# Kernel tuning notes

Measured on AMD Instinct MI355X. Metric: run time of the kernel, lower is better.

The kernel has to match this reference:

```python
import jax, jax.numpy as jnp
import numpy as np

VAR = (0.1, 0.2)        # SSD encoding variances
THRESH = 0.5            # overlap_thresh
NEGPOS = 3              # neg:pos ratio


def _point_form(p):
    # (cx,cy,w,h) -> (x1,y1,x2,y2)
    return jnp.concatenate([p[:, :2] - p[:, 2:] / 2, p[:, :2] + p[:, 2:] / 2], axis=1)


def _jaccard(a, b):
    # a: [O,4], b: [P,4], corner form -> IoU [O,P]
    lt = jnp.maximum(a[:, None, :2], b[None, :, :2])
    rb = jnp.minimum(a[:, None, 2:], b[None, :, 2:])
    wh = jnp.maximum(rb - lt, 0.0)
    inter = wh[..., 0] * wh[..., 1]
    area_a = ((a[:, 2] - a[:, 0]) * (a[:, 3] - a[:, 1]))[:, None]
    area_b = ((b[:, 2] - b[:, 0]) * (b[:, 3] - b[:, 1]))[None, :]
    return inter / (area_a + area_b - inter)


def _encode(matched, priors):
    # matched: [P,4] corner form, priors: [P,4] center form
    g_cxcy = ((matched[:, :2] + matched[:, 2:]) / 2 - priors[:, :2]) / (VAR[0] * priors[:, 2:])
    g_wh = jnp.log((matched[:, 2:] - matched[:, :2]) / priors[:, 2:]) / VAR[1]
    return jnp.concatenate([g_cxcy, g_wh], axis=1)


def _match(truths, labels, priors):
    # truths: [O,4], labels: [O], priors: [P,4] -> loc_t [P,4], conf_t [P], obj_t [P]
    O = truths.shape[0]
    over = _jaccard(truths, _point_form(priors))          # [O,P]
    best_prior_idx = jnp.argmax(over, axis=1)             # [O] best prior per truth
    best_truth_overlap = over.max(axis=0)                 # [P]
    best_truth_idx = jnp.argmax(over, axis=0)             # [P]
    best_truth_overlap = best_truth_overlap.at[best_prior_idx].set(2.0)
    best_truth_idx = best_truth_idx.at[best_prior_idx].set(jnp.arange(O))
    matched = truths[best_truth_idx]                      # [P,4]
    conf = labels[best_truth_idx].astype(jnp.int32) + 1   # background = 0
    conf = jnp.where(best_truth_overlap < THRESH, 0, conf)
    return _encode(matched, priors), conf, conf > 0


def _ce(logits, tgt):
    # per-element cross entropy, logits [...,C], tgt [...] int
    return jax.nn.logsumexp(logits, axis=-1) - jnp.take_along_axis(logits, tgt[..., None], axis=-1)[..., 0]


def _mine_neg(loss, pos, P):
    # hard negative mining via double argsort (rank of each elem in descending loss order)
    loss = jnp.where(pos, 0.0, loss)
    loss_idx = jnp.argsort(-loss, axis=1)
    idx_rank = jnp.argsort(loss_idx, axis=1)
    num_neg = jnp.minimum(NEGPOS * pos.sum(axis=1, keepdims=True), P - 1)
    return idx_rank < num_neg


def setup_inputs() -> dict:
    key = jax.random.key(0)
    ks = jax.random.split(key, 8)
    B, P, C, O = 64, 16320, 81, 50
    loc_data = jax.random.normal(ks[0], (B, P, 4), jnp.float32)
    conf_data = jax.random.normal(ks[1], (B, P, C), jnp.float32)
    obj_data = jax.random.normal(ks[2], (B, P, 2), jnp.float32)
    # priors: center form, positive w/h
    cxcy = jax.random.uniform(ks[3], (P, 2), minval=0.05, maxval=0.95)
    wh = jax.random.uniform(ks[4], (P, 2), minval=0.02, maxval=0.3)
    priors = jnp.concatenate([cxcy, wh], axis=1).astype(jnp.float32)
    # targets: valid corner-form boxes + float label in last column
    tc = jax.random.uniform(ks[5], (B, O, 2), minval=0.1, maxval=0.9)
    twh = jax.random.uniform(ks[6], (B, O, 2), minval=0.05, maxval=0.3)
    boxes = jnp.concatenate([jnp.clip(tc - twh / 2, 0.0, 1.0), jnp.clip(tc + twh / 2, 0.0, 1.0)], axis=-1)
    labels = jax.random.randint(ks[7], (B, O), 0, C).astype(jnp.float32)
    targets = jnp.concatenate([boxes, labels[..., None]], axis=-1).astype(jnp.float32)
    return {"loc_data": loc_data, "conf_data": conf_data, "obj_data": obj_data,
            "priors": priors, "targets": targets}


def reference(loc_data, conf_data, obj_data, priors, targets):
    B, P, C = conf_data.shape
    loc_t, conf_t, pos = jax.vmap(lambda t: _match(t[:, :4], t[:, 4], priors))(targets)
    loc_t = jax.lax.stop_gradient(loc_t)  # torch builds targets detached

    # localization: smooth L1 over positives, sum reduction
    d = loc_data - loc_t
    sl1 = jnp.where(jnp.abs(d) < 1.0, 0.5 * d * d, jnp.abs(d) - 0.5)
    loss_l = jnp.sum(sl1 * pos[..., None].astype(sl1.dtype))

    # combined (C+1)-way logit: col0 = obj_bg + log(sum(exp(conf))), cols 1..C = obj_fg + conf
    lse_conf = jax.nn.logsumexp(conf_data, axis=-1)                        # [B,P]
    logit = jnp.concatenate([(obj_data[..., 0] + lse_conf)[..., None],
                             obj_data[..., 1:2] + conf_data], axis=-1)     # [B,P,C+1]

    ce_c = _ce(logit, conf_t)                       # [B,P]
    neg_c = _mine_neg(ce_c, pos, P)
    loss_c = jnp.sum(jnp.where(pos | neg_c, ce_c, 0.0))

    ce_o = _ce(obj_data, pos.astype(jnp.int32))     # [B,P]
    neg_o = _mine_neg(ce_o, pos, P)
    loss_obj = jnp.sum(jnp.where(pos | neg_o, ce_o, 0.0))

    N = pos.sum().astype(jnp.float32)
    return loss_l / N, loss_c / N, loss_obj / N
```

## Files before the change

### kernel.cpp

```cpp
#include <hip/hip_runtime.h>
#include <cstdint>
#include <cstddef>

#define THRESH   0.5f
#define NEGPOS   3
#define VAR0     0.1f
#define VAR1     0.2f
#define MAXO     64
#define NPRI     8
#define A1_T     256
#define MINE_T   1024
#define MINE_W   (MINE_T / 64)
#define HCOPIES  8

__global__ __launch_bounds__(A1_T)
void match_kernel(const float* __restrict__ priors,
                  const float* __restrict__ targets,
                  unsigned char* __restrict__ code,
                  unsigned long long* __restrict__ g_bp,
                  int B, int P, int O, int chunks) {
    __shared__ float tx1[MAXO], ty1[MAXO], tx2[MAXO], ty2[MAXO], tarea[MAXO];
    const int b   = blockIdx.x / chunks;
    const int ch  = blockIdx.x % chunks;
    const int tid = threadIdx.x;

    if (tid < O) {
        const float* tr = targets + (size_t)(b * O + tid) * 5;
        float x1 = tr[0], y1 = tr[1], x2 = tr[2], y2 = tr[3];
        tx1[tid] = x1; ty1[tid] = y1; tx2[tid] = x2; ty2[tid] = y2;
        tarea[tid] = (x2 - x1) * (y2 - y1);
    }
    __syncthreads();

    float px1[NPRI], py1[NPRI], px2[NPRI], py2[NPRI], pa[NPRI], pov[NPRI];
    int   pidx[NPRI];
    const int p0 = ch * (A1_T * NPRI) + tid;
#pragma unroll
    for (int i = 0; i < NPRI; ++i) {
        int p = p0 + i * A1_T;
        pov[i] = -1.0f; pidx[i] = 0;
        px1[i] = 0.f; py1[i] = 0.f; px2[i] = 0.f; py2[i] = 0.f; pa[i] = 1.0f;
        if (p < P) {
            float4 pr = *(const float4*)(priors + (size_t)p * 4);
            px1[i] = pr.x - pr.z * 0.5f; py1[i] = pr.y - pr.w * 0.5f;
            px2[i] = pr.x + pr.z * 0.5f; py2[i] = pr.y + pr.w * 0.5f;
            pa[i]  = pr.z * pr.w;
        }
    }

    const int lane = tid & 63;
    for (int o = 0; o < O; ++o) {
        float ax1 = tx1[o], ay1 = ty1[o], ax2 = tx2[o], ay2 = ty2[o], aa = tarea[o];
        float bo = -1.0f; unsigned bp = 0u;
#pragma unroll
        for (int i = 0; i < NPRI; ++i) {
            float lx = fmaxf(ax1, px1[i]), ly = fmaxf(ay1, py1[i]);
            float rx = fminf(ax2, px2[i]), ry = fminf(ay2, py2[i]);
            float w = fmaxf(rx - lx, 0.0f), h = fmaxf(ry - ly, 0.0f);
            float inter = w * h;
            float iou = __fdividef(inter, aa + pa[i] - inter);
            if (iou > pov[i]) { pov[i] = iou; pidx[i] = o; }
            if (iou > bo)     { bo = iou; bp = (unsigned)(p0 + i * A1_T); }
        }
        unsigned long long key =
            ((unsigned long long)__float_as_uint(bo) << 32) |
            (unsigned long long)(0xFFFFFFFFu - bp);
#pragma unroll
        for (int d = 1; d < 64; d <<= 1) {
            unsigned long long other = __shfl_xor(key, d, 64);
            if (other > key) key = other;
        }
        if (lane == 0)
            atomicMax(&g_bp[(size_t)b * O + o], key);
    }

#pragma unroll
    for (int i = 0; i < NPRI; ++i) {
        int p = p0 + i * A1_T;
        if (p < P)
            code[(size_t)b * P + p] =
                (pov[i] >= THRESH) ? (unsigned char)(pidx[i] + 1) : (unsigned char)0;
    }
}

__global__ void force_kernel(const unsigned long long* __restrict__ g_bp,
                             unsigned char* __restrict__ code,
                             int B, int P, int O) {
    int b = blockIdx.x * blockDim.x + threadIdx.x;
    if (b >= B) return;
    for (int o = 0; o < O; ++o) {
        unsigned long long key = g_bp[(size_t)b * O + o];
        unsigned p = 0xFFFFFFFFu - (unsigned)(key & 0xFFFFFFFFull);
        code[(size_t)b * P + p] = (unsigned char)(o + 1);
    }
}

__global__ __launch_bounds__(256)
void ce_pos_kernel(const float* __restrict__ loc, const float* __restrict__ conf,
                   const float* __restrict__ obj, const float* __restrict__ priors,
                   const float* __restrict__ targets,
                   const unsigned char* __restrict__ code,
                   float* __restrict__ mce, float* __restrict__ rowacc,
                   int B, int P, int C, int O) {
    const int b = blockIdx.y;
    const int p = blockIdx.x * 256 + threadIdx.x;
    const int tid = threadIdx.x, wv = tid >> 6, lane = tid & 63;

    bool pos = false;
    unsigned cc = 0;
    const unsigned t = (unsigned)(b * P + p);
    float obx = 0.f, oby = 0.f, lse2 = 0.f;
    if (p < P) {
        cc = code[t];
        float2 ob = *(const float2*)(obj + (size_t)t * 2);
        obx = ob.x; oby = ob.y;
        float m = fmaxf(obx, oby);
        lse2 = m + __logf(__expf(obx - m) + __expf(oby - m));
        if (cc == 0) {
            mce[t] = lse2 - obx;
        } else {
            mce[t] = 0.0f;
            pos = true;
        }
    }

    const unsigned long long msk = __ballot(pos);
    float myS = 0.f;
    unsigned long long rem = msk;
    while (rem) {
        const int src = __ffsll(rem) - 1;
        rem &= rem - 1;
        const unsigned t_s = (unsigned)__shfl((int)t, src, 64);
        const float* cr = conf + (size_t)t_s * C;
        float s = 0.f;
        for (int j = lane; j < C; j += 64) s += __expf(cr[j]);
#pragma unroll
        for (int d = 1; d < 64; d <<= 1) s += __shfl_xor(s, d, 64);
        if (lane == src) myS = s;
    }

    float sl = 0.f, cec = 0.f, ceo = 0.f;
    if (pos) {
        const float* cr = conf + (size_t)t * C;
        const float* tr = targets + (size_t)((unsigned)(b * O) + cc - 1u) * 5;
        float4 pr = *(const float4*)(priors + (size_t)p * 4);
        float4 ld = *(const float4*)(loc + (size_t)t * 4);
        float mx1 = tr[0], my1 = tr[1], mx2 = tr[2], my2 = tr[3];
        int   lbl = (int)tr[4];

        float lsec = __logf(myS);
        cec = lsec + lse2 - oby - cr[lbl];
        ceo = lse2 - oby;

        float gx  = ((mx1 + mx2) * 0.5f - pr.x) / (VAR0 * pr.z);
        float gy  = ((my1 + my2) * 0.5f - pr.y) / (VAR0 * pr.w);
        float gw2 = __logf((mx2 - mx1) / pr.z) / VAR1;
        float gh  = __logf((my2 - my1) / pr.w) / VAR1;
        float d0 = ld.x - gx,  a0 = fabsf(d0); sl += (a0 < 1.f) ? 0.5f * d0 * d0 : a0 - 0.5f;
        float d1 = ld.y - gy,  a1 = fabsf(d1); sl += (a1 < 1.f) ? 0.5f * d1 * d1 : a1 - 0.5f;
        float d2 = ld.z - gw2, a2 = fabsf(d2); sl += (a2 < 1.f) ? 0.5f * d2 * d2 : a2 - 0.5f;
        float d3 = ld.w - gh,  a3 = fabsf(d3); sl += (a3 < 1.f) ? 0.5f * d3 * d3 : a3 - 0.5f;
    }

    float cntp = (float)__popcll(msk);
    __shared__ float red[4][4];
#pragma unroll
    for (int d = 32; d > 0; d >>= 1) {
        sl  += __shfl_down(sl,  d, 64);
        cec += __shfl_down(cec, d, 64);
        ceo += __shfl_down(ceo, d, 64);
    }
    if (lane == 0) {
        red[wv][0] = cntp; red[wv][1] = sl; red[wv][2] = cec; red[wv][3] = ceo;
    }
    __syncthreads();
    if (tid < 4) {
        float v = red[0][tid] + red[1][tid] + red[2][tid] + red[3][tid];
        if (v != 0.0f)
            atomicAdd(rowacc + (size_t)b * 16 + tid, v);
    }
}

__global__ __launch_bounds__(MINE_T)
void mine_kernel(const float* __restrict__ mce, const float* __restrict__ rowacc,
                 float* __restrict__ g_neg, int P) {
    const int b = blockIdx.x;
    const float* row = mce + (size_t)b * P;
    int npos = (int)rowacc[(size_t)b * 16];
    int k = NEGPOS * npos;
    if (k > P - 1) k = P - 1;
    if (k <= 0) return;

    __shared__ unsigned hist[HCOPIES][257];
    __shared__ unsigned s_prefix;
    __shared__ int      s_rem;
    __shared__ float    s_ws[MINE_W];
    __shared__ int      s_wc[MINE_W];

    const int tid  = threadIdx.x;
    const int wv   = tid >> 6;
    const int hc   = wv & (HCOPIES - 1);
    const int lane = tid & 63;

    unsigned prefix = 0u;
    int rem = k;
    for (int shift = 24; shift >= 0; shift -= 8) {
        for (int i = tid; i < HCOPIES * 257; i += MINE_T) (&hist[0][0])[i] = 0u;
        __syncthreads();
        unsigned himask = (shift == 24) ? 0u : (0xFFFFFFFFu << (shift + 8));
        for (int i = tid; i < P; i += MINE_T) {
            unsigned bits = __float_as_uint(row[i]);
            if ((bits & himask) == prefix)
                atomicAdd(&hist[hc][(bits >> shift) & 0xFFu], 1u);
        }
        __syncthreads();
        if (tid == 0) {
            int cum = 0; unsigned bin = 0;
            for (int bb = 255; bb >= 0; --bb) {
                int cnt = 0;
#pragma unroll
                for (int h = 0; h < HCOPIES; ++h) cnt += (int)hist[h][bb];
                if (cum + cnt >= rem) { bin = (unsigned)bb; rem -= cum; break; }
                cum += cnt;
            }
            s_prefix = prefix | (bin << shift);
            s_rem = rem;
        }
        __syncthreads();
        prefix = s_prefix;
        rem    = s_rem;
    }

    float vk = __uint_as_float(prefix);
    float s = 0.f; int cnt = 0;
    for (int i = tid; i < P; i += MINE_T) {
        float v = row[i];
        if (__float_as_uint(v) > prefix) { s += v; ++cnt; }
    }
#pragma unroll
    for (int d = 32; d > 0; d >>= 1) {
        s   += __shfl_down(s, d, 64);
        cnt += __shfl_down(cnt, d, 64);
    }
    if (lane == 0) { s_ws[wv] = s; s_wc[wv] = cnt; }
    __syncthreads();
    if (tid == 0) {
        float st = 0.f; int ct = 0;
        for (int w = 0; w < MINE_W; ++w) { st += s_ws[w]; ct += s_wc[w]; }
        atomicAdd(g_neg, st + (float)(k - ct) * vk);
    }
}

__global__ void finish_kernel(const float* __restrict__ rowacc,
                              const float* __restrict__ g_neg,
                              float* __restrict__ out, int B) {
    const int lane = threadIdx.x;
    float npos = 0.f, sl = 0.f, cec = 0.f, ceo = 0.f;
    for (int b = lane; b < B; b += 64) {
        float4 v = *(const float4*)(rowacc + (size_t)b * 16);
        npos += v.x; sl += v.y; cec += v.z; ceo += v.w;
    }
#pragma unroll
    for (int d = 32; d > 0; d >>= 1) {
        npos += __shfl_down(npos, d, 64);
        sl   += __shfl_down(sl,   d, 64);
        cec  += __shfl_down(cec,  d, 64);
        ceo  += __shfl_down(ceo,  d, 64);
    }
    if (lane == 0) {
        float neg = *g_neg;
        out[0] = sl / npos;
        out[1] = (cec + neg) / npos;
        out[2] = (ceo + neg) / npos;
    }
}

extern "C" void kernel_launch(void* const* d_in, const int* in_sizes, int n_in,
                              void* d_out, int out_size, void* d_ws, size_t ws_size,
                              hipStream_t stream) {
    const float* loc     = (const float*)d_in[0];
    const float* conf    = (const float*)d_in[1];
    const float* obj     = (const float*)d_in[2];
    const float* priors  = (const float*)d_in[3];
    const float* targets = (const float*)d_in[4];

    const int P = in_sizes[3] / 4;
    const int B = in_sizes[0] / (4 * P);
    const int C = in_sizes[1] / (B * P);
    const int O = in_sizes[4] / (5 * B);

    char* ws = (char*)d_ws;
    size_t off = 0;
    float* g_neg = (float*)(ws + off);             off += 64;
    float* rowacc = (float*)(ws + off);            off += (size_t)B * 16 * sizeof(float);
    unsigned long long* g_bp = (unsigned long long*)(ws + off);
    off += (size_t)B * O * sizeof(unsigned long long);
    const size_t zero_bytes = off;
    off = (off + 127) & ~(size_t)127;
    unsigned char* code = (unsigned char*)(ws + off); off += (size_t)B * P;
    off = (off + 127) & ~(size_t)127;
    float* mce = (float*)(ws + off);               off += (size_t)B * P * sizeof(float);

    hipMemsetAsync(d_ws, 0, zero_bytes, stream);

    const int chunks = (P + A1_T * NPRI - 1) / (A1_T * NPRI);
    match_kernel<<<B * chunks, A1_T, 0, stream>>>(priors, targets, code, g_bp,
                                                  B, P, O, chunks);
    force_kernel<<<(B + 63) / 64, 64, 0, stream>>>(g_bp, code, B, P, O);
    dim3 ce_grid((P + 255) / 256, B);
    ce_pos_kernel<<<ce_grid, 256, 0, stream>>>(loc, conf, obj, priors, targets,
                                               code, mce, rowacc, B, P, C, O);
    mine_kernel<<<B, MINE_T, 0, stream>>>(mce, rowacc, g_neg, P);
    finish_kernel<<<1, 64, 0, stream>>>(rowacc, g_neg, (float*)d_out, B);
}
```

Before: 587.5 us.

## Fuse CE/positive pass with hard-negative mining in one per-row block

Merges the per-prior cross-entropy/positive-loss kernel and the radix-select mining kernel into one kernel with one 1024-thread block per batch row, keeping the mined losses in registers instead of writing and rereading them from global memory. It also parallelizes the force-match step per target with duplicate resolution, and replaces the serial bin scan in the radix select with a wave prefix scan. Per-row results go straight into rowacc instead of through atomics. The cost is much less parallelism in the CE stage (B blocks instead of B×P/256), and it caps P at 16K priors per row.

```diff
diff --git a/kernel.cpp b/kernel.cpp
--- a/kernel.cpp
+++ b/kernel.cpp
@@ -9,9 +9,9 @@
 #define MAXO     64
 #define NPRI     8
 #define A1_T     256
-#define MINE_T   1024
-#define MINE_W   (MINE_T / 64)
-#define HCOPIES  8
+#define FUSED_T  1024
+#define FWAVES   (FUSED_T / 64)
+#define MAXCH    16
 
 __global__ __launch_bounds__(A1_T)
 void match_kernel(const float* __restrict__ priors,
@@ -83,87 +83,100 @@
     }
 }
 
-__global__ void force_kernel(const unsigned long long* __restrict__ g_bp,
-                             unsigned char* __restrict__ code,
-                             int B, int P, int O) {
-    int b = blockIdx.x * blockDim.x + threadIdx.x;
-    if (b >= B) return;
-    for (int o = 0; o < O; ++o) {
-        unsigned long long key = g_bp[(size_t)b * O + o];
-        unsigned p = 0xFFFFFFFFu - (unsigned)(key & 0xFFFFFFFFull);
-        code[(size_t)b * P + p] = (unsigned char)(o + 1);
-    }
-}
-
-__global__ __launch_bounds__(256)
-void ce_pos_kernel(const float* __restrict__ loc, const float* __restrict__ conf,
-                   const float* __restrict__ obj, const float* __restrict__ priors,
-                   const float* __restrict__ targets,
-                   const unsigned char* __restrict__ code,
-                   float* __restrict__ mce, float* __restrict__ rowacc,
-                   int B, int P, int C, int O) {
-    const int b = blockIdx.y;
-    const int p = blockIdx.x * 256 + threadIdx.x;
+__global__ __launch_bounds__(64)
+void force_kernel(const unsigned long long* __restrict__ g_bp,
+                  unsigned char* __restrict__ code,
+                  int B, int P, int O) {
+    const int b = blockIdx.x;
+    const int o = threadIdx.x;
+    __shared__ unsigned sp[MAXO];
+    if (o < O)
+        sp[o] = 0xFFFFFFFFu - (unsigned)(g_bp[(size_t)b * O + o] & 0xFFFFFFFFull);
+    __syncthreads();
+    if (o < O) {
+        unsigned p = sp[o];
+        bool win = true;
+        for (int o2 = o + 1; o2 < O; ++o2)
+            if (sp[o2] == p) { win = false; break; }
+        if (win)
+            code[(size_t)b * P + p] = (unsigned char)(o + 1);
+    }
+}
+
+__global__ __launch_bounds__(FUSED_T)
+void fused_kernel(const float* __restrict__ loc, const float* __restrict__ conf,
+                  const float* __restrict__ obj, const float* __restrict__ priors,
+                  const float* __restrict__ targets,
+                  const unsigned char* __restrict__ code,
+                  float* __restrict__ rowacc,
+                  int B, int P, int C, int O) {
+    const int b = blockIdx.x;
     const int tid = threadIdx.x, wv = tid >> 6, lane = tid & 63;
 
-    bool pos = false;
-    unsigned cc = 0;
-    const unsigned t = (unsigned)(b * P + p);
-    float obx = 0.f, oby = 0.f, lse2 = 0.f;
-    if (p < P) {
-        cc = code[t];
-        float2 ob = *(const float2*)(obj + (size_t)t * 2);
-        obx = ob.x; oby = ob.y;
-        float m = fmaxf(obx, oby);
-        lse2 = m + __logf(__expf(obx - m) + __expf(oby - m));
-        if (cc == 0) {
-            mce[t] = lse2 - obx;
-        } else {
-            mce[t] = 0.0f;
-            pos = true;
-        }
-    }
-
-    const unsigned long long msk = __ballot(pos);
-    float myS = 0.f;
-    unsigned long long rem = msk;
-    while (rem) {
-        const int src = __ffsll(rem) - 1;
-        rem &= rem - 1;
-        const unsigned t_s = (unsigned)__shfl((int)t, src, 64);
-        const float* cr = conf + (size_t)t_s * C;
-        float s = 0.f;
-        for (int j = lane; j < C; j += 64) s += __expf(cr[j]);
-#pragma unroll
-        for (int d = 1; d < 64; d <<= 1) s += __shfl_xor(s, d, 64);
-        if (lane == src) myS = s;
-    }
-
+    float r[MAXCH];
     float sl = 0.f, cec = 0.f, ceo = 0.f;
-    if (pos) {
-        const float* cr = conf + (size_t)t * C;
-        const float* tr = targets + (size_t)((unsigned)(b * O) + cc - 1u) * 5;
-        float4 pr = *(const float4*)(priors + (size_t)p * 4);
-        float4 ld = *(const float4*)(loc + (size_t)t * 4);
-        float mx1 = tr[0], my1 = tr[1], mx2 = tr[2], my2 = tr[3];
-        int   lbl = (int)tr[4];
-
-        float lsec = __logf(myS);
-        cec = lsec + lse2 - oby - cr[lbl];
-        ceo = lse2 - oby;
-
-        float gx  = ((mx1 + mx2) * 0.5f - pr.x) / (VAR0 * pr.z);
-        float gy  = ((my1 + my2) * 0.5f - pr.y) / (VAR0 * pr.w);
-        float gw2 = __logf((mx2 - mx1) / pr.z) / VAR1;
-        float gh  = __logf((my2 - my1) / pr.w) / VAR1;
-        float d0 = ld.x - gx,  a0 = fabsf(d0); sl += (a0 < 1.f) ? 0.5f * d0 * d0 : a0 - 0.5f;
-        float d1 = ld.y - gy,  a1 = fabsf(d1); sl += (a1 < 1.f) ? 0.5f * d1 * d1 : a1 - 0.5f;
-        float d2 = ld.z - gw2, a2 = fabsf(d2); sl += (a2 < 1.f) ? 0.5f * d2 * d2 : a2 - 0.5f;
-        float d3 = ld.w - gh,  a3 = fabsf(d3); sl += (a3 < 1.f) ? 0.5f * d3 * d3 : a3 - 0.5f;
-    }
-
-    float cntp = (float)__popcll(msk);
-    __shared__ float red[4][4];
+    int cntp = 0;
+
+#pragma unroll
+    for (int i = 0; i < MAXCH; ++i) {
+        const int p = i * FUSED_T + tid;
+        const unsigned t = (unsigned)(b * P + p);
+        bool pos = false;
+        unsigned cc = 0;
+        float oby = 0.f, lse2 = 0.f;
+        r[i] = 0.f;
+        if (p < P) {
+            cc = code[t];
+            float2 ob = *(const float2*)(obj + (size_t)t * 2);
+            float m = fmaxf(ob.x, ob.y);
+            lse2 = m + __logf(__expf(ob.x - m) + __expf(ob.y - m));
+            oby = ob.y;
+            if (cc == 0) r[i] = lse2 - ob.x;
+            else         pos = true;
+        }
+
+        const unsigned long long msk = __ballot(pos);
+        cntp += __popcll(msk);
+
+        float myS = 0.f;
+        unsigned long long remb = msk;
+        while (remb) {
+            const int src = __ffsll(remb) - 1;
+            remb &= remb - 1;
+            const unsigned t_s = (unsigned)__shfl((int)t, src, 64);
+            const float* cr = conf + (size_t)t_s * C;
+            float s = 0.f;
+            for (int j = lane; j < C; j += 64) s += __expf(cr[j]);
+#pragma unroll
+            for (int d = 1; d < 64; d <<= 1) s += __shfl_xor(s, d, 64);
+            if (lane == src) myS = s;
+        }
+
+        if (pos) {
+            const float* cr = conf + (size_t)t * C;
+            const float* tr = targets + (size_t)((unsigned)(b * O) + cc - 1u) * 5;
+            float4 pr = *(const float4*)(priors + (size_t)p * 4);
+            float4 ld = *(const float4*)(loc + (size_t)t * 4);
+            float mx1 = tr[0], my1 = tr[1], mx2 = tr[2], my2 = tr[3];
+            int   lbl = (int)tr[4];
+
+            float lsec = __logf(myS);
+            cec += lsec + lse2 - oby - cr[lbl];
+            ceo += lse2 - oby;
+
+            float gx  = ((mx1 + mx2) * 0.5f - pr.x) / (VAR0 * pr.z);
+            float gy  = ((my1 + my2) * 0.5f - pr.y) / (VAR0 * pr.w);
+            float gw2 = __logf((mx2 - mx1) / pr.z) / VAR1;
+            float gh  = __logf((my2 - my1) / pr.w) / VAR1;
+            float d0 = ld.x - gx,  a0 = fabsf(d0); sl += (a0 < 1.f) ? 0.5f * d0 * d0 : a0 - 0.5f;
+            float d1 = ld.y - gy,  a1 = fabsf(d1); sl += (a1 < 1.f) ? 0.5f * d1 * d1 : a1 - 0.5f;
+            float d2 = ld.z - gw2, a2 = fabsf(d2); sl += (a2 < 1.f) ? 0.5f * d2 * d2 : a2 - 0.5f;
+            float d3 = ld.w - gh,  a3 = fabsf(d3); sl += (a3 < 1.f) ? 0.5f * d3 * d3 : a3 - 0.5f;
+        }
+    }
+
+    __shared__ float red[FWAVES][4];
+    __shared__ int s_npos;
 #pragma unroll
     for (int d = 32; d > 0; d >>= 1) {
         sl  += __shfl_down(sl,  d, 64);
@@ -171,70 +184,83 @@
         ceo += __shfl_down(ceo, d, 64);
     }
     if (lane == 0) {
-        red[wv][0] = cntp; red[wv][1] = sl; red[wv][2] = cec; red[wv][3] = ceo;
+        red[wv][0] = (float)cntp; red[wv][1] = sl; red[wv][2] = cec; red[wv][3] = ceo;
     }
     __syncthreads();
     if (tid < 4) {
-        float v = red[0][tid] + red[1][tid] + red[2][tid] + red[3][tid];
-        if (v != 0.0f)
-            atomicAdd(rowacc + (size_t)b * 16 + tid, v);
-    }
-}
-
-__global__ __launch_bounds__(MINE_T)
-void mine_kernel(const float* __restrict__ mce, const float* __restrict__ rowacc,
-                 float* __restrict__ g_neg, int P) {
-    const int b = blockIdx.x;
-    const float* row = mce + (size_t)b * P;
-    int npos = (int)rowacc[(size_t)b * 16];
-    int k = NEGPOS * npos;
+        float v = 0.f;
+        for (int w = 0; w < FWAVES; ++w) v += red[w][tid];
+        rowacc[(size_t)b * 16 + tid] = v;
+        if (tid == 0) s_npos = (int)v;
+    }
+    __syncthreads();
+
+    int k = NEGPOS * s_npos;
     if (k > P - 1) k = P - 1;
-    if (k <= 0) return;
-
-    __shared__ unsigned hist[HCOPIES][257];
+    if (k <= 0) {
+        if (tid == 0) rowacc[(size_t)b * 16 + 4] = 0.f;
+        return;
+    }
+
+    __shared__ unsigned hist[FWAVES][257];
+    __shared__ unsigned binc[256];
     __shared__ unsigned s_prefix;
     __shared__ int      s_rem;
-    __shared__ float    s_ws[MINE_W];
-    __shared__ int      s_wc[MINE_W];
-
-    const int tid  = threadIdx.x;
-    const int wv   = tid >> 6;
-    const int hc   = wv & (HCOPIES - 1);
-    const int lane = tid & 63;
 
     unsigned prefix = 0u;
     int rem = k;
     for (int shift = 24; shift >= 0; shift -= 8) {
-        for (int i = tid; i < HCOPIES * 257; i += MINE_T) (&hist[0][0])[i] = 0u;
+        for (int i = tid; i < FWAVES * 257; i += FUSED_T) (&hist[0][0])[i] = 0u;
         __syncthreads();
-        unsigned himask = (shift == 24) ? 0u : (0xFFFFFFFFu << (shift + 8));
-        for (int i = tid; i < P; i += MINE_T) {
-            unsigned bits = __float_as_uint(row[i]);
+        const unsigned himask = (shift == 24) ? 0u : (0xFFFFFFFFu << (shift + 8));
+#pragma unroll
+        for (int i = 0; i < MAXCH; ++i) {
+            unsigned bits = __float_as_uint(r[i]);
             if ((bits & himask) == prefix)
-                atomicAdd(&hist[hc][(bits >> shift) & 0xFFu], 1u);
+                atomicAdd(&hist[wv][(bits >> shift) & 0xFFu], 1u);
         }
         __syncthreads();
-        if (tid == 0) {
-            int cum = 0; unsigned bin = 0;
-            for (int bb = 255; bb >= 0; --bb) {
-                int cnt = 0;
-#pragma unroll
-                for (int h = 0; h < HCOPIES; ++h) cnt += (int)hist[h][bb];
-                if (cum + cnt >= rem) { bin = (unsigned)bb; rem -= cum; break; }
-                cum += cnt;
+        if (tid < 256) {
+            unsigned c = 0;
+            for (int h = 0; h < FWAVES; ++h) c += hist[h][tid];
+            binc[tid] = c;
+        }
+        __syncthreads();
+        if (tid < 64) {
+            const int bb0 = 255 - 4 * tid;
+            unsigned c0 = binc[bb0], c1 = binc[bb0 - 1],
+                     c2 = binc[bb0 - 2], c3 = binc[bb0 - 3];
+            unsigned t4 = c0 + c1 + c2 + c3;
+            unsigned incl = t4;
+#pragma unroll
+            for (int d = 1; d < 64; d <<= 1) {
+                unsigned v = __shfl_up(incl, d, 64);
+                if (tid >= d) incl += v;
             }
-            s_prefix = prefix | (bin << shift);
-            s_rem = rem;
+            const unsigned excl = incl - t4;
+            if ((int)excl < rem && rem <= (int)incl) {
+                unsigned cum = excl;
+                int bin, nrem;
+                if ((int)(cum + c0) >= rem)      { bin = bb0;     nrem = rem - (int)cum; }
+                else { cum += c0;
+                if ((int)(cum + c1) >= rem)      { bin = bb0 - 1; nrem = rem - (int)cum; }
+                else { cum += c1;
+                if ((int)(cum + c2) >= rem)      { bin = bb0 - 2; nrem = rem - (int)cum; }
+                else { cum += c2;                  bin = bb0 - 3; nrem = rem - (int)cum; } } }
+                s_prefix = prefix | ((unsigned)bin << shift);
+                s_rem    = nrem;
+            }
         }
         __syncthreads();
         prefix = s_prefix;
         rem    = s_rem;
     }
 
-    float vk = __uint_as_float(prefix);
+    const float vk = __uint_as_float(prefix);
     float s = 0.f; int cnt = 0;
-    for (int i = tid; i < P; i += MINE_T) {
-        float v = row[i];
+#pragma unroll
+    for (int i = 0; i < MAXCH; ++i) {
+        float v = r[i];
         if (__float_as_uint(v) > prefix) { s += v; ++cnt; }
     }
 #pragma unroll
@@ -242,23 +268,26 @@
         s   += __shfl_down(s, d, 64);
         cnt += __shfl_down(cnt, d, 64);
     }
+    __shared__ float s_ws[FWAVES];
+    __shared__ int   s_wc[FWAVES];
     if (lane == 0) { s_ws[wv] = s; s_wc[wv] = cnt; }
     __syncthreads();
     if (tid == 0) {
         float st = 0.f; int ct = 0;
-        for (int w = 0; w < MINE_W; ++w) { st += s_ws[w]; ct += s_wc[w]; }
-        atomicAdd(g_neg, st + (float)(k - ct) * vk);
-    }
-}
-
-__global__ void finish_kernel(const float* __restrict__ rowacc,
-                              const float* __restrict__ g_neg,
-                              float* __restrict__ out, int B) {
+        for (int w = 0; w < FWAVES; ++w) { st += s_ws[w]; ct += s_wc[w]; }
+        rowacc[(size_t)b * 16 + 4] = st + (float)(k - ct) * vk;
+    }
+}
+
+__global__ __launch_bounds__(64)
+void finish_kernel(const float* __restrict__ rowacc,
+                   float* __restrict__ out, int B) {
     const int lane = threadIdx.x;
-    float npos = 0.f, sl = 0.f, cec = 0.f, ceo = 0.f;
+    float npos = 0.f, sl = 0.f, cec = 0.f, ceo = 0.f, neg = 0.f;
     for (int b = lane; b < B; b += 64) {
-        float4 v = *(const float4*)(rowacc + (size_t)b * 16);
-        npos += v.x; sl += v.y; cec += v.z; ceo += v.w;
+        const float* rb = rowacc + (size_t)b * 16;
+        float4 v = *(const float4*)rb;
+        npos += v.x; sl += v.y; cec += v.z; ceo += v.w; neg += rb[4];
     }
 #pragma unroll
     for (int d = 32; d > 0; d >>= 1) {
@@ -266,9 +295,9 @@
         sl   += __shfl_down(sl,   d, 64);
         cec  += __shfl_down(cec,  d, 64);
         ceo  += __shfl_down(ceo,  d, 64);
+        neg  += __shfl_down(neg,  d, 64);
     }
     if (lane == 0) {
-        float neg = *g_neg;
         out[0] = sl / npos;
         out[1] = (cec + neg) / npos;
         out[2] = (ceo + neg) / npos;
@@ -291,25 +320,20 @@
 
     char* ws = (char*)d_ws;
     size_t off = 0;
-    float* g_neg = (float*)(ws + off);             off += 64;
-    float* rowacc = (float*)(ws + off);            off += (size_t)B * 16 * sizeof(float);
     unsigned long long* g_bp = (unsigned long long*)(ws + off);
     off += (size_t)B * O * sizeof(unsigned long long);
     const size_t zero_bytes = off;
+    float* rowacc = (float*)(ws + off);            off += (size_t)B * 16 * sizeof(float);
     off = (off + 127) & ~(size_t)127;
     unsigned char* code = (unsigned char*)(ws + off); off += (size_t)B * P;
-    off = (off + 127) & ~(size_t)127;
-    float* mce = (float*)(ws + off);               off += (size_t)B * P * sizeof(float);
 
     hipMemsetAsync(d_ws, 0, zero_bytes, stream);
 
     const int chunks = (P + A1_T * NPRI - 1) / (A1_T * NPRI);
     match_kernel<<<B * chunks, A1_T, 0, stream>>>(priors, targets, code, g_bp,
                                                   B, P, O, chunks);
-    force_kernel<<<(B + 63) / 64, 64, 0, stream>>>(g_bp, code, B, P, O);
-    dim3 ce_grid((P + 255) / 256, B);
-    ce_pos_kernel<<<ce_grid, 256, 0, stream>>>(loc, conf, obj, priors, targets,
-                                               code, mce, rowacc, B, P, C, O);
-    mine_kernel<<<B, MINE_T, 0, stream>>>(mce, rowacc, g_neg, P);
-    finish_kernel<<<1, 64, 0, stream>>>(rowacc, g_neg, (float*)d_out, B);
-}
+    force_kernel<<<B, 64, 0, stream>>>(g_bp, code, B, P, O);
+    fused_kernel<<<B, FUSED_T, 0, stream>>>(loc, conf, obj, priors, targets,
+                                            code, rowacc, B, P, C, O);
+    finish_kernel<<<1, 64, 0, stream>>>(rowacc, (float*)d_out, B);
+}
```

Measured after the change: 645.9 us. +10.0%, slower.

## Parallelize force-match per truth and radix-select bin scan in mining

Applied to the files above, without the earlier changes.

The force-match kernel now uses one block per image, with one thread per truth. A later truth that maps to the same prior overrides an earlier one, which keeps the sequential last-write-wins semantics. The mining kernel caches each row in registers (up to 16 values per thread) instead of re-reading global memory on every radix pass. It gives each wave its own histogram copy and replaces the single-thread 256-bin scan with a parallel reduce and wave prefix scan. The register cache assumes P <= 16*1024; larger P would silently drop elements.

```diff
diff --git a/kernel.cpp b/kernel.cpp
--- a/kernel.cpp
+++ b/kernel.cpp
@@ -11,7 +11,7 @@
 #define A1_T     256
 #define MINE_T   1024
 #define MINE_W   (MINE_T / 64)
-#define HCOPIES  8
+#define MINE_CH  16
 
 __global__ __launch_bounds__(A1_T)
 void match_kernel(const float* __restrict__ priors,
@@ -83,15 +83,23 @@
     }
 }
 
-__global__ void force_kernel(const unsigned long long* __restrict__ g_bp,
-                             unsigned char* __restrict__ code,
-                             int B, int P, int O) {
-    int b = blockIdx.x * blockDim.x + threadIdx.x;
-    if (b >= B) return;
-    for (int o = 0; o < O; ++o) {
-        unsigned long long key = g_bp[(size_t)b * O + o];
-        unsigned p = 0xFFFFFFFFu - (unsigned)(key & 0xFFFFFFFFull);
-        code[(size_t)b * P + p] = (unsigned char)(o + 1);
+__global__ __launch_bounds__(64)
+void force_kernel(const unsigned long long* __restrict__ g_bp,
+                  unsigned char* __restrict__ code,
+                  int B, int P, int O) {
+    const int b = blockIdx.x;
+    const int o = threadIdx.x;
+    __shared__ unsigned sp[MAXO];
+    if (o < O)
+        sp[o] = 0xFFFFFFFFu - (unsigned)(g_bp[(size_t)b * O + o] & 0xFFFFFFFFull);
+    __syncthreads();
+    if (o < O) {
+        unsigned p = sp[o];
+        bool win = true;
+        for (int o2 = o + 1; o2 < O; ++o2)
+            if (sp[o2] == p) { win = false; break; }
+        if (win)
+            code[(size_t)b * P + p] = (unsigned char)(o + 1);
     }
 }
 
@@ -191,50 +199,77 @@
     if (k > P - 1) k = P - 1;
     if (k <= 0) return;
 
-    __shared__ unsigned hist[HCOPIES][257];
+    const int tid  = threadIdx.x;
+    const int wv   = tid >> 6;
+    const int lane = tid & 63;
+
+    float r[MINE_CH];
+#pragma unroll
+    for (int i = 0; i < MINE_CH; ++i) {
+        const int p = i * MINE_T + tid;
+        r[i] = (p < P) ? row[p] : 0.0f;
+    }
+
+    __shared__ unsigned hist[MINE_W][257];
+    __shared__ unsigned binc[256];
     __shared__ unsigned s_prefix;
     __shared__ int      s_rem;
-    __shared__ float    s_ws[MINE_W];
-    __shared__ int      s_wc[MINE_W];
-
-    const int tid  = threadIdx.x;
-    const int wv   = tid >> 6;
-    const int hc   = wv & (HCOPIES - 1);
-    const int lane = tid & 63;
 
     unsigned prefix = 0u;
     int rem = k;
     for (int shift = 24; shift >= 0; shift -= 8) {
-        for (int i = tid; i < HCOPIES * 257; i += MINE_T) (&hist[0][0])[i] = 0u;
+        for (int i = tid; i < MINE_W * 257; i += MINE_T) (&hist[0][0])[i] = 0u;
         __syncthreads();
-        unsigned himask = (shift == 24) ? 0u : (0xFFFFFFFFu << (shift + 8));
-        for (int i = tid; i < P; i += MINE_T) {
-            unsigned bits = __float_as_uint(row[i]);
+        const unsigned himask = (shift == 24) ? 0u : (0xFFFFFFFFu << (shift + 8));
+#pragma unroll
+        for (int i = 0; i < MINE_CH; ++i) {
+            unsigned bits = __float_as_uint(r[i]);
             if ((bits & himask) == prefix)
-                atomicAdd(&hist[hc][(bits >> shift) & 0xFFu], 1u);
+                atomicAdd(&hist[wv][(bits >> shift) & 0xFFu], 1u);
         }
         __syncthreads();
-        if (tid == 0) {
-            int cum = 0; unsigned bin = 0;
-            for (int bb = 255; bb >= 0; --bb) {
-                int cnt = 0;
-#pragma unroll
-                for (int h = 0; h < HCOPIES; ++h) cnt += (int)hist[h][bb];
-                if (cum + cnt >= rem) { bin = (unsigned)bb; rem -= cum; break; }
-                cum += cnt;
+        if (tid < 256) {
+            unsigned c = 0;
+#pragma unroll
+            for (int h = 0; h < MINE_W; ++h) c += hist[h][tid];
+            binc[tid] = c;
+        }
+        __syncthreads();
+        if (tid < 64) {
+            const int bb0 = 255 - 4 * tid;
+            unsigned c0 = binc[bb0], c1 = binc[bb0 - 1],
+                     c2 = binc[bb0 - 2], c3 = binc[bb0 - 3];
+            unsigned t4 = c0 + c1 + c2 + c3;
+            unsigned incl = t4;
+#pragma unroll
+            for (int d = 1; d < 64; d <<= 1) {
+                unsigned v = __shfl_up(incl, d, 64);
+                if (tid >= d) incl += v;
             }
-            s_prefix = prefix | (bin << shift);
-            s_rem = rem;
+            const unsigned excl = incl - t4;
+            if ((int)excl < rem && rem <= (int)incl) {
+                unsigned cum = excl;
+                int bin, nrem;
+                if ((int)(cum + c0) >= rem)      { bin = bb0;     nrem = rem - (int)cum; }
+                else { cum += c0;
+                if ((int)(cum + c1) >= rem)      { bin = bb0 - 1; nrem = rem - (int)cum; }
+                else { cum += c1;
+                if ((int)(cum + c2) >= rem)      { bin = bb0 - 2; nrem = rem - (int)cum; }
+                else { cum += c2;                  bin = bb0 - 3; nrem = rem - (int)cum; } } }
+                s_prefix = prefix | ((unsigned)bin << shift);
+                s_rem    = nrem;
+            }
         }
         __syncthreads();
         prefix = s_prefix;
         rem    = s_rem;
     }
 
-    float vk = __uint_as_float(prefix);
+    const float vk = __uint_as_float(prefix);
     float s = 0.f; int cnt = 0;
-    for (int i = tid; i < P; i += MINE_T) {
-        float v = row[i];
+#pragma unroll
+    for (int i = 0; i < MINE_CH; ++i) {
+        float v = r[i];
         if (__float_as_uint(v) > prefix) { s += v; ++cnt; }
     }
 #pragma unroll
@@ -242,6 +277,8 @@
         s   += __shfl_down(s, d, 64);
         cnt += __shfl_down(cnt, d, 64);
     }
+    __shared__ float s_ws[MINE_W];
+    __shared__ int   s_wc[MINE_W];
     if (lane == 0) { s_ws[wv] = s; s_wc[wv] = cnt; }
     __syncthreads();
     if (tid == 0) {
@@ -251,9 +288,10 @@
     }
 }
 
-__global__ void finish_kernel(const float* __restrict__ rowacc,
-                              const float* __restrict__ g_neg,
-                              float* __restrict__ out, int B) {
+__global__ __launch_bounds__(64)
+void finish_kernel(const float* __restrict__ rowacc,
+                   const float* __restrict__ g_neg,
+                   float* __restrict__ out, int B) {
     const int lane = threadIdx.x;
     float npos = 0.f, sl = 0.f, cec = 0.f, ceo = 0.f;
     for (int b = lane; b < B; b += 64) {
@@ -306,7 +344,7 @@
     const int chunks = (P + A1_T * NPRI - 1) / (A1_T * NPRI);
     match_kernel<<<B * chunks, A1_T, 0, stream>>>(priors, targets, code, g_bp,
                                                   B, P, O, chunks);
-    force_kernel<<<(B + 63) / 64, 64, 0, stream>>>(g_bp, code, B, P, O);
+    force_kernel<<<B, 64, 0, stream>>>(g_bp, code, B, P, O);
     dim3 ce_grid((P + 255) / 256, B);
     ce_pos_kernel<<<ce_grid, 256, 0, stream>>>(loc, conf, obj, priors, targets,
                                                code, mce, rowacc, B, P, C, O);
```

Result: faster. 511.2 us (-13.0%).
